# Kernel tuning notes

Hardware: AMD Instinct MI355X
Metric: run time of the kernel (lower is better)

The kernel has to match this reference:

```python
import jax, jax.numpy as jnp
import numpy as np
from jax import lax

WIN = 9  # window side length (default [9]*ndims in the torch module)


def _box_sum3d(x, win):
    # x: [C, 1, D, H, W]; sliding-window sum with zero padding == conv3d with
    return lax.reduce_window(
        x, jnp.array(0, x.dtype), lax.add,
        window_dimensions=(1, 1, win, win, win),
        window_strides=(1, 1, 1, 1, 1),
        padding='SAME')


def setup_inputs() -> dict:
    key = jax.random.key(0)
    k1, k2 = jax.random.split(key)
    shape = (1, 2, 192, 224, 192)  # [batch, channel, D, H, W]
    y_pred = jax.random.uniform(k1, shape, dtype=jnp.float32)
    y_true = jax.random.uniform(k2, shape, dtype=jnp.float32)
    return {"y_pred": y_pred, "y_true": y_true}


def reference(y_pred, y_true):
    # permute(1, 0, 2, 3, 4): [B, C, D, H, W] -> [C, B, D, H, W]
    Ii = jnp.transpose(y_pred, (1, 0, 2, 3, 4))
    Ji = jnp.transpose(y_true, (1, 0, 2, 3, 4))
    win_size = jnp.array(WIN ** 3, Ii.dtype)

    I_sum = _box_sum3d(Ii, WIN)
    J_sum = _box_sum3d(Ji, WIN)
    I2_sum = _box_sum3d(Ii * Ii, WIN)
    J2_sum = _box_sum3d(Ji * Ji, WIN)
    IJ_sum = _box_sum3d(Ii * Ji, WIN)

    u_I = I_sum / win_size
    u_J = J_sum / win_size

    cross = IJ_sum - u_J * I_sum - u_I * J_sum + u_I * u_J * win_size
    I_var = I2_sum - 2 * u_I * I_sum + u_I * u_I * win_size
    J_var = J2_sum - 2 * u_J * J_sum + u_J * u_J * win_size

    cc = cross * cross / (I_var * J_var + 1e-5)
    return -jnp.mean(cc)
```

## Files before the change

kernel.cpp:

```cpp
#include <hip/hip_runtime.h>
#include <hip/hip_fp16.h>


#define C2   2
#define DDIM 192
#define HDIM 224
#define WDIM 192
#define HWN  (HDIM*WDIM)
#define VOL  ((size_t)DDIM*HWN)
#define RAD  4
#define WINV (1.0f/729.0f)

#define HT1  28
#define NROW 204

__global__ __launch_bounds__(256, 3)
void k_hwsum(const float* __restrict__ I, const float* __restrict__ J,
             __half* __restrict__ buf, int d0, int dbeg, int dend, int bufD)
{
    const int tid = threadIdx.x;
    const int wv  = tid >> 6;
    const int l   = tid & 63;
    const int w0  = 3 * l;
    int d = dbeg + 4*blockIdx.x + wv;
    if (d >= dend) d = dend - 1;
    const int h0 = blockIdx.y * HT1;
    const int c  = blockIdx.z;

    __shared__ float wrow[4][5][NROW];

    if (l < 4) {
        #pragma unroll
        for (int f = 0; f < 5; ++f) wrow[wv][f][l] = 0.f;
    }
    if (l < 8) {
        #pragma unroll
        for (int f = 0; f < 5; ++f) wrow[wv][f][196 + l] = 0.f;
    }

    const float* Ib = I + (size_t)c*VOL + (size_t)d*HWN + w0;
    const float* Jb = J + (size_t)c*VOL + (size_t)d*HWN + w0;

    float3 ringI[9], ringJ[9];
    float3 rs[5];
    #pragma unroll
    for (int f = 0; f < 5; ++f) { rs[f].x = 0.f; rs[f].y = 0.f; rs[f].z = 0.f; }

    #pragma unroll
    for (int k = 0; k < 8; ++k) {
        const int h = h0 - RAD + k;
        float3 iv = {0.f,0.f,0.f}, jv = {0.f,0.f,0.f};
        if (h >= 0 && h < HDIM) {
            iv = *(const float3*)(Ib + (size_t)h*WDIM);
            jv = *(const float3*)(Jb + (size_t)h*WDIM);
        }
        ringI[k] = iv; ringJ[k] = jv;
        rs[0].x += iv.x;      rs[0].y += iv.y;      rs[0].z += iv.z;
        rs[1].x += jv.x;      rs[1].y += jv.y;      rs[1].z += jv.z;
        rs[2].x += iv.x*iv.x; rs[2].y += iv.y*iv.y; rs[2].z += iv.z*iv.z;
        rs[3].x += jv.x*jv.x; rs[3].y += jv.y*jv.y; rs[3].z += jv.z*jv.z;
        rs[4].x += iv.x*jv.x; rs[4].y += iv.y*jv.y; rs[4].z += iv.z*jv.z;
    }

    float3 niv = {0.f,0.f,0.f}, njv = {0.f,0.f,0.f};
    {
        const int hf = h0 + RAD;
        if (hf < HDIM) {
            niv = *(const float3*)(Ib + (size_t)hf*WDIM);
            njv = *(const float3*)(Jb + (size_t)hf*WDIM);
        }
    }

    const size_t fstride = (size_t)C2*bufD*HWN;
    __half* ob = buf + ((size_t)c*bufD + (size_t)(d - d0 + RAD))*HWN + w0;
    float* const rowp = &wrow[wv][0][0];

    int i = 0;
    while (i < HT1) {
        #pragma unroll
        for (int p9 = 0; p9 < 9; ++p9) {
            if (i < HT1) {
                const int h = h0 + i;
                const float3 iv = niv, jv = njv;
                niv.x=0.f; niv.y=0.f; niv.z=0.f; njv.x=0.f; njv.y=0.f; njv.z=0.f;
                const int hf2 = h + 1 + RAD;
                if (i + 1 < HT1 && hf2 < HDIM) {
                    niv = *(const float3*)(Ib + (size_t)hf2*WDIM);
                    njv = *(const float3*)(Jb + (size_t)hf2*WDIM);
                }
                rs[0].x += iv.x;      rs[0].y += iv.y;      rs[0].z += iv.z;
                rs[1].x += jv.x;      rs[1].y += jv.y;      rs[1].z += jv.z;
                rs[2].x += iv.x*iv.x; rs[2].y += iv.y*iv.y; rs[2].z += iv.z*iv.z;
                rs[3].x += jv.x*jv.x; rs[3].y += jv.y*jv.y; rs[3].z += jv.z*jv.z;
                rs[4].x += iv.x*jv.x; rs[4].y += iv.y*jv.y; rs[4].z += iv.z*jv.z;
                #pragma unroll
                for (int f = 0; f < 5; ++f) {
                    float* q = rowp + f*NROW + 4 + w0;
                    q[0] = rs[f].x; q[1] = rs[f].y; q[2] = rs[f].z;
                }
                {
                    const float3 ri = ringI[p9], rj = ringJ[p9];
                    rs[0].x -= ri.x;      rs[0].y -= ri.y;      rs[0].z -= ri.z;
                    rs[1].x -= rj.x;      rs[1].y -= rj.y;      rs[1].z -= rj.z;
                    rs[2].x -= ri.x*ri.x; rs[2].y -= ri.y*ri.y; rs[2].z -= ri.z*ri.z;
                    rs[3].x -= rj.x*rj.x; rs[3].y -= rj.y*rj.y; rs[3].z -= rj.z*rj.z;
                    rs[4].x -= ri.x*rj.x; rs[4].y -= ri.y*rj.y; rs[4].z -= ri.z*rj.z;
                    ringI[(p9+8)%9] = iv; ringJ[(p9+8)%9] = jv;
                }
                asm volatile("s_waitcnt lgkmcnt(0)" ::: "memory");
                #pragma unroll
                for (int f = 0; f < 5; ++f) {
                    const float* q = rowp + f*NROW + 3*l;
                    const float a0=q[0], a1=q[1], a2=q[2], a3=q[3], a4=q[4];
                    const float a5=q[5], a6=q[6], a7=q[7], a8=q[8], a9=q[9], a10=q[10];
                    const float o0 = ((a0+a1)+(a2+a3)) + ((a4+a5)+(a6+a7)) + a8;
                    const float o1 = o0 - a0 + a9;
                    const float o2 = o1 - a1 + a10;
                    __half* pf = ob + f*fstride + (size_t)h*WDIM;
                    *reinterpret_cast<__half2*>(pf) = __floats2half2_rn(o0, o1);
                    pf[2] = __float2half_rn(o2);
                }
                ++i;
            }
        }
    }
}

__global__ __launch_bounds__(256)
void k_dsum(const __half* __restrict__ buf, double* __restrict__ gacc,
            int d0, int bufD, int DS)
{
    const int tid = threadIdx.x;
    const int pix = blockIdx.x*256 + tid;
    const int c   = blockIdx.z;
    const int ds0 = d0 + blockIdx.y*DS;

    const size_t fstride = (size_t)C2*bufD*HWN;
    const __half* base = buf + (size_t)c*bufD*HWN + pix;

    float ring[5][9];
    float rs[5] = {0.f,0.f,0.f,0.f,0.f};
    float acc = 0.f;

    #pragma unroll
    for (int k = 0; k < 8; ++k) {
        const int dd = ds0 - RAD + k;
        float v[5] = {0.f,0.f,0.f,0.f,0.f};
        if ((unsigned)dd < (unsigned)DDIM) {
            const __half* pp = base + (size_t)(dd - d0 + RAD)*HWN;
            #pragma unroll
            for (int f = 0; f < 5; ++f) v[f] = __half2float(pp[(size_t)f*fstride]);
        }
        #pragma unroll
        for (int f = 0; f < 5; ++f) { ring[f][k] = v[f]; rs[f] += v[f]; }
    }

    int i = 0;
    while (i < DS) {
        #pragma unroll
        for (int p = 0; p < 9; ++p) {
            if (i < DS) {
                const int dd = ds0 + i + RAD;
                float v[5] = {0.f,0.f,0.f,0.f,0.f};
                if (dd < DDIM) {
                    const __half* pp = base + (size_t)(dd - d0 + RAD)*HWN;
                    #pragma unroll
                    for (int f = 0; f < 5; ++f) v[f] = __half2float(pp[(size_t)f*fstride]);
                }
                float S[5];
                #pragma unroll
                for (int f = 0; f < 5; ++f) {
                    rs[f] += v[f];
                    S[f] = rs[f];
                    rs[f] -= ring[f][p];
                    ring[f][(p+8)%9] = v[f];
                }
                const float uI    = S[0]*WINV;
                const float uJ    = S[1]*WINV;
                const float cross = S[4] - uJ*S[0];
                const float Iv    = S[2] - uI*S[0];
                const float Jv    = S[3] - uJ*S[1];
                acc += cross*cross / (Iv*Jv + 1e-5f);
                ++i;
            }
        }
    }

    __shared__ float wred[4];
    #pragma unroll
    for (int off = 32; off > 0; off >>= 1) acc += __shfl_down(acc, off);
    if ((tid & 63) == 0) wred[tid >> 6] = acc;
    __syncthreads();
    if (tid == 0) {
        const float sum = wred[0] + wred[1] + wred[2] + wred[3];
        atomicAdd(gacc, (double)sum);
    }
}

__global__ void k_fin(const double* __restrict__ gacc, float* __restrict__ out)
{
    out[0] = (float)(-gacc[0] / (double)((size_t)C2*DDIM*HDIM*WDIM));
}

extern "C" void kernel_launch(void* const* d_in, const int* in_sizes, int n_in,
                              void* d_out, int out_size, void* d_ws, size_t ws_size,
                              hipStream_t stream)
{
    if (n_in < 2) return;
    const float* I = (const float*)d_in[0];
    const float* J = (const float*)d_in[1];
    float* out = (float*)d_out;
    double* gacc = (double*)d_ws;
    __half* buf = (__half*)((char*)d_ws + 256);

    static const int cands[] = {192, 96, 48, 24, 12, 6, 4, 2, 1};
    int Dc = 0;
    for (int c : cands) {
        const size_t need = 256 + (size_t)5*C2*(c+8)*HWN*sizeof(__half);
        if (need <= ws_size) { Dc = c; break; }
    }
    if (Dc == 0) return;

    hipMemsetAsync(d_ws, 0, 256, stream);

    const int DS   = (Dc % 48 == 0) ? 48 : Dc;
    const int nsub = Dc / DS;
    const int bufD = Dc + 8;

    for (int d0 = 0; d0 < DDIM; d0 += Dc) {
        const int dbeg = (d0 - RAD < 0) ? 0 : d0 - RAD;
        const int dend = (d0 + Dc + RAD > DDIM) ? DDIM : d0 + Dc + RAD;
        const int nd   = dend - dbeg;
        dim3 g1((nd + 3)/4, HDIM/HT1, C2);
        k_hwsum<<<g1, dim3(256,1,1), 0, stream>>>(I, J, buf, d0, dbeg, dend, bufD);
        dim3 g2(HWN/256, nsub, C2);
        k_dsum<<<g2, dim3(256,1,1), 0, stream>>>(buf, gacc, d0, bufD, DS);
    }
    k_fin<<<1,1,0,stream>>>(gacc, out);
}
```

Measured before the change: 123.0 us.

## Replace LDS W-window sum with wave shuffles and reload trailing rows

```diff
diff --git a/kernel.cpp b/kernel.cpp
--- a/kernel.cpp
+++ b/kernel.cpp
@@ -11,10 +11,9 @@
 #define RAD  4
 #define WINV (1.0f/729.0f)
 
-#define HT1  28
-#define NROW 204
-
-__global__ __launch_bounds__(256, 3)
+#define HT1  14
+
+__global__ __launch_bounds__(256, 5)
 void k_hwsum(const float* __restrict__ I, const float* __restrict__ J,
              __half* __restrict__ buf, int d0, int dbeg, int dend, int bufD)
 {
@@ -27,102 +26,96 @@
     const int h0 = blockIdx.y * HT1;
     const int c  = blockIdx.z;
 
-    __shared__ float wrow[4][5][NROW];
-
-    if (l < 4) {
-        #pragma unroll
-        for (int f = 0; f < 5; ++f) wrow[wv][f][l] = 0.f;
-    }
-    if (l < 8) {
-        #pragma unroll
-        for (int f = 0; f < 5; ++f) wrow[wv][f][196 + l] = 0.f;
-    }
-
     const float* Ib = I + (size_t)c*VOL + (size_t)d*HWN + w0;
     const float* Jb = J + (size_t)c*VOL + (size_t)d*HWN + w0;
 
-    float3 ringI[9], ringJ[9];
-    float3 rs[5];
-    #pragma unroll
-    for (int f = 0; f < 5; ++f) { rs[f].x = 0.f; rs[f].y = 0.f; rs[f].z = 0.f; }
+    float3 rs0{0,0,0}, rs1{0,0,0}, rs2{0,0,0}, rs3{0,0,0}, rs4{0,0,0};
 
     #pragma unroll
     for (int k = 0; k < 8; ++k) {
         const int h = h0 - RAD + k;
-        float3 iv = {0.f,0.f,0.f}, jv = {0.f,0.f,0.f};
+        float3 iv{0,0,0}, jv{0,0,0};
         if (h >= 0 && h < HDIM) {
             iv = *(const float3*)(Ib + (size_t)h*WDIM);
             jv = *(const float3*)(Jb + (size_t)h*WDIM);
         }
-        ringI[k] = iv; ringJ[k] = jv;
-        rs[0].x += iv.x;      rs[0].y += iv.y;      rs[0].z += iv.z;
-        rs[1].x += jv.x;      rs[1].y += jv.y;      rs[1].z += jv.z;
-        rs[2].x += iv.x*iv.x; rs[2].y += iv.y*iv.y; rs[2].z += iv.z*iv.z;
-        rs[3].x += jv.x*jv.x; rs[3].y += jv.y*jv.y; rs[3].z += jv.z*jv.z;
-        rs[4].x += iv.x*jv.x; rs[4].y += iv.y*jv.y; rs[4].z += iv.z*jv.z;
-    }
-
-    float3 niv = {0.f,0.f,0.f}, njv = {0.f,0.f,0.f};
+        rs0.x += iv.x;      rs0.y += iv.y;      rs0.z += iv.z;
+        rs1.x += jv.x;      rs1.y += jv.y;      rs1.z += jv.z;
+        rs2.x += iv.x*iv.x; rs2.y += iv.y*iv.y; rs2.z += iv.z*iv.z;
+        rs3.x += jv.x*jv.x; rs3.y += jv.y*jv.y; rs3.z += jv.z*jv.z;
+        rs4.x += iv.x*jv.x; rs4.y += iv.y*jv.y; rs4.z += iv.z*jv.z;
+    }
+
+    float3 nai{0,0,0}, naj{0,0,0}, ndi{0,0,0}, ndj{0,0,0};
     {
-        const int hf = h0 + RAD;
-        if (hf < HDIM) {
-            niv = *(const float3*)(Ib + (size_t)hf*WDIM);
-            njv = *(const float3*)(Jb + (size_t)hf*WDIM);
+        const int ha = h0 + RAD;
+        nai = *(const float3*)(Ib + (size_t)ha*WDIM);
+        naj = *(const float3*)(Jb + (size_t)ha*WDIM);
+        const int hd = h0 - RAD;
+        if (hd >= 0) {
+            ndi = *(const float3*)(Ib + (size_t)hd*WDIM);
+            ndj = *(const float3*)(Jb + (size_t)hd*WDIM);
         }
     }
 
     const size_t fstride = (size_t)C2*bufD*HWN;
     __half* ob = buf + ((size_t)c*bufD + (size_t)(d - d0 + RAD))*HWN + w0;
-    float* const rowp = &wrow[wv][0][0];
-
-    int i = 0;
-    while (i < HT1) {
-        #pragma unroll
-        for (int p9 = 0; p9 < 9; ++p9) {
-            if (i < HT1) {
-                const int h = h0 + i;
-                const float3 iv = niv, jv = njv;
-                niv.x=0.f; niv.y=0.f; niv.z=0.f; njv.x=0.f; njv.y=0.f; njv.z=0.f;
-                const int hf2 = h + 1 + RAD;
-                if (i + 1 < HT1 && hf2 < HDIM) {
-                    niv = *(const float3*)(Ib + (size_t)hf2*WDIM);
-                    njv = *(const float3*)(Jb + (size_t)hf2*WDIM);
-                }
-                rs[0].x += iv.x;      rs[0].y += iv.y;      rs[0].z += iv.z;
-                rs[1].x += jv.x;      rs[1].y += jv.y;      rs[1].z += jv.z;
-                rs[2].x += iv.x*iv.x; rs[2].y += iv.y*iv.y; rs[2].z += iv.z*iv.z;
-                rs[3].x += jv.x*jv.x; rs[3].y += jv.y*jv.y; rs[3].z += jv.z*jv.z;
-                rs[4].x += iv.x*jv.x; rs[4].y += iv.y*jv.y; rs[4].z += iv.z*jv.z;
-                #pragma unroll
-                for (int f = 0; f < 5; ++f) {
-                    float* q = rowp + f*NROW + 4 + w0;
-                    q[0] = rs[f].x; q[1] = rs[f].y; q[2] = rs[f].z;
-                }
-                {
-                    const float3 ri = ringI[p9], rj = ringJ[p9];
-                    rs[0].x -= ri.x;      rs[0].y -= ri.y;      rs[0].z -= ri.z;
-                    rs[1].x -= rj.x;      rs[1].y -= rj.y;      rs[1].z -= rj.z;
-                    rs[2].x -= ri.x*ri.x; rs[2].y -= ri.y*ri.y; rs[2].z -= ri.z*ri.z;
-                    rs[3].x -= rj.x*rj.x; rs[3].y -= rj.y*rj.y; rs[3].z -= rj.z*rj.z;
-                    rs[4].x -= ri.x*rj.x; rs[4].y -= ri.y*rj.y; rs[4].z -= ri.z*rj.z;
-                    ringI[(p9+8)%9] = iv; ringJ[(p9+8)%9] = jv;
-                }
-                asm volatile("s_waitcnt lgkmcnt(0)" ::: "memory");
-                #pragma unroll
-                for (int f = 0; f < 5; ++f) {
-                    const float* q = rowp + f*NROW + 3*l;
-                    const float a0=q[0], a1=q[1], a2=q[2], a3=q[3], a4=q[4];
-                    const float a5=q[5], a6=q[6], a7=q[7], a8=q[8], a9=q[9], a10=q[10];
-                    const float o0 = ((a0+a1)+(a2+a3)) + ((a4+a5)+(a6+a7)) + a8;
-                    const float o1 = o0 - a0 + a9;
-                    const float o2 = o1 - a1 + a10;
-                    __half* pf = ob + f*fstride + (size_t)h*WDIM;
-                    *reinterpret_cast<__half2*>(pf) = __floats2half2_rn(o0, o1);
-                    pf[2] = __float2half_rn(o2);
-                }
-                ++i;
+
+    const bool m1m = (l >= 1), m2m = (l >= 2);
+    const bool m1p = (l <= 62), m2p = (l <= 61);
+
+    for (int i = 0; i < HT1; ++i) {
+        const int h = h0 + i;
+        const float3 ai = nai, aj = naj, di = ndi, dj = ndj;
+
+        nai = {0,0,0}; naj = {0,0,0}; ndi = {0,0,0}; ndj = {0,0,0};
+        if (i + 1 < HT1) {
+            const int ha = h + 1 + RAD;
+            if (ha < HDIM) {
+                nai = *(const float3*)(Ib + (size_t)ha*WDIM);
+                naj = *(const float3*)(Jb + (size_t)ha*WDIM);
             }
-        }
+            const int hd = h + 1 - RAD;
+            if (hd >= 0) {
+                ndi = *(const float3*)(Ib + (size_t)hd*WDIM);
+                ndj = *(const float3*)(Jb + (size_t)hd*WDIM);
+            }
+        }
+
+        rs0.x += ai.x;      rs0.y += ai.y;      rs0.z += ai.z;
+        rs1.x += aj.x;      rs1.y += aj.y;      rs1.z += aj.z;
+        rs2.x += ai.x*ai.x; rs2.y += ai.y*ai.y; rs2.z += ai.z*ai.z;
+        rs3.x += aj.x*aj.x; rs3.y += aj.y*aj.y; rs3.z += aj.z*aj.z;
+        rs4.x += ai.x*aj.x; rs4.y += ai.y*aj.y; rs4.z += ai.z*aj.z;
+
+        #define WSUM_STORE(RS, F)                                            \
+        {                                                                    \
+            const float T = RS.x + RS.y + RS.z;                              \
+            float Tm  = __shfl(T,    l-1); Tm  = m1m ? Tm  : 0.f;            \
+            float Tp  = __shfl(T,    l+1); Tp  = m1p ? Tp  : 0.f;            \
+            float z2m = __shfl(RS.z, l-2); z2m = m2m ? z2m : 0.f;            \
+            float z1p = __shfl(RS.z, l+1); z1p = m1p ? z1p : 0.f;            \
+            float x1m = __shfl(RS.x, l-1); x1m = m1m ? x1m : 0.f;            \
+            float x2p = __shfl(RS.x, l+2); x2p = m2p ? x2p : 0.f;            \
+            const float o1 = Tm + T + Tp;                                    \
+            const float o0 = o1 + z2m - z1p;                                 \
+            const float o2 = o1 - x1m + x2p;                                 \
+            __half* pf = ob + (size_t)F*fstride + (size_t)h*WDIM;            \
+            *reinterpret_cast<__half2*>(pf) = __floats2half2_rn(o0, o1);     \
+            pf[2] = __float2half_rn(o2);                                     \
+        }
+        WSUM_STORE(rs0, 0)
+        WSUM_STORE(rs1, 1)
+        WSUM_STORE(rs2, 2)
+        WSUM_STORE(rs3, 3)
+        WSUM_STORE(rs4, 4)
+        #undef WSUM_STORE
+
+        rs0.x -= di.x;      rs0.y -= di.y;      rs0.z -= di.z;
+        rs1.x -= dj.x;      rs1.y -= dj.y;      rs1.z -= dj.z;
+        rs2.x -= di.x*di.x; rs2.y -= di.y*di.y; rs2.z -= di.z*di.z;
+        rs3.x -= dj.x*dj.x; rs3.y -= dj.y*dj.y; rs3.z -= dj.z*dj.z;
+        rs4.x -= di.x*dj.x; rs4.y -= di.y*dj.y; rs4.z -= di.z*dj.z;
     }
 }
 
```

Result: slower. 146.3 us (+19.0%).
